# Kernel tuning notes

Measured on AMD Instinct MI355X. Metric: run time of the kernel, lower is better.

The kernel has to match this reference:

```python
import jax, jax.numpy as jnp
import numpy as np

N_HEAD = 16
D_K = 64


def _bn(x, g, b, eps=1e-5):
    # torch BatchNorm1d in training mode: biased batch variance
    m = jnp.mean(x, axis=0)
    v = jnp.var(x, axis=0)
    return (x - m) * jax.lax.rsqrt(v + eps) * g + b


def setup_inputs() -> dict:
    key = jax.random.key(0)
    ks = jax.random.split(key, 8)
    B, DX, NK, DKIN, H, DK, DO = 128, 1024, 1024, 512, N_HEAD, D_K, 512
    sc = 0.02
    return {
        "x": jax.random.normal(ks[0], (B, DX), dtype=jnp.float32),
        "k": jax.random.normal(ks[1], (B, NK, DKIN), dtype=jnp.float32),
        "bn1_g": jnp.ones((DX,), jnp.float32),
        "bn1_b": jnp.zeros((DX,), jnp.float32),
        "Wx": jax.random.normal(ks[2], (H * DK, DX), dtype=jnp.float32) * sc,
        "bx": jnp.zeros((H * DK,), jnp.float32),
        "Wk": jax.random.normal(ks[3], (H * DK, DKIN), dtype=jnp.float32) * sc,
        "bk": jnp.zeros((H * DK,), jnp.float32),
        "bn2_g": jnp.ones((DK,), jnp.float32),
        "bn2_b": jnp.zeros((DK,), jnp.float32),
        "Wlin": jax.random.normal(ks[4], (DK, DK), dtype=jnp.float32) * sc,
        "blin": jnp.zeros((DK,), jnp.float32),
        "Wo": jax.random.normal(ks[5], (DO, H * DK), dtype=jnp.float32) * sc,
        "bo": jnp.zeros((DO,), jnp.float32),
    }


def reference(x, k, bn1_g, bn1_b, Wx, bx, Wk, bk, bn2_g, bn2_b, Wlin, blin, Wo, bo):
    H, DK = N_HEAD, D_K
    B, DX = x.shape
    NK = k.shape[1]
    # outer BN + query projection (n_x == 1)
    xq = _bn(x, bn1_g, bn1_b) @ Wx.T + bx                     # (B, H*DK)
    xq = xq.reshape(B, H, DK).transpose(1, 0, 2).reshape(H * B, DK)
    kp = (k @ Wk.T + bk).reshape(B, NK, H, DK)
    kp = kp.transpose(2, 0, 1, 3).reshape(H * B, NK, DK)       # (H*B, NK, DK)
    # inner CrossAttention: BN + linear on the single query vector
    latent = _bn(xq, bn2_g, bn2_b) @ Wlin.T + blin             # (H*B, DK)
    u = jnp.einsum('bnd,bd->bn', kp, latent)                   # (H*B, NK)
    # softmax over the singleton query dim (dim=2) -> all ones, kept faithful
    attn = jax.nn.softmax(u[..., None], axis=-1)[..., 0]       # (H*B, NK)
    out = jnp.einsum('bnd,bn->bd', kp, attn)                   # (H*B, DK)
    out = out.reshape(H, B, DK).transpose(1, 0, 2).reshape(B, H * DK)
    x_hid = latent.reshape(H, B, DK).transpose(1, 0, 2).reshape(B, H * DK)
    # attn.view(n_head, batch, d_x_).permute(1,2,0).contiguous().view(batch, n_head, -1)
    attn_out = attn.reshape(H, B, NK).transpose(1, 2, 0).reshape(B, H, -1)
    return (attn_out, out @ Wo.T + bo, x_hid @ Wo.T + bo)
```

## Files before the change

### kernel.cpp

```cpp
#include <hip/hip_runtime.h>

typedef __attribute__((ext_vector_type(8))) short short8;
typedef __attribute__((ext_vector_type(4))) float floatx4;

__device__ __forceinline__ unsigned short f2bf(float f) {
    unsigned int x = __float_as_uint(f);
    x = x + 0x7FFFu + ((x >> 16) & 1u);
    return (unsigned short)(x >> 16);
}

template <typename OutT, bool STATS>
__device__ __forceinline__ void gemm_tile(
    const unsigned short* __restrict__ A, int lda,
    const unsigned short* __restrict__ B, int ldb,
    const float* __restrict__ bias, float bscale,
    OutT* __restrict__ C, int ldc, int tilesN, int K, int wave, int lane,
    float* sS, float* sSS)
{
    int tm = wave / tilesN, tn = wave % tilesN;
    int mn = lane & 15, q = lane >> 4;
    const short8* ap = (const short8*)(A + (size_t)(tm * 16 + mn) * lda + q * 8);
    const short8* bp = (const short8*)(B + (size_t)(tn * 16 + mn) * ldb + q * 8);
    floatx4 acc = {0.f, 0.f, 0.f, 0.f};
    #pragma unroll 4
    for (int k = 0; k < K; k += 32) {
        short8 a = *ap; ap += 4;
        short8 b = *bp; bp += 4;
        acc = __builtin_amdgcn_mfma_f32_16x16x32_bf16(a, b, acc, 0, 0, 0);
    }
    int col = tn * 16 + mn;
    float bv = bias[col] * bscale;
    float lsum = 0.f, lss = 0.f;
    #pragma unroll
    for (int r = 0; r < 4; ++r) {
        int row = tm * 16 + q * 4 + r;
        float v = acc[r] + bv;
        OutT* dst = C + (size_t)row * ldc + col;
        if constexpr (sizeof(OutT) == 2) *dst = (OutT)f2bf(v);
        else                             *dst = (OutT)v;
        if constexpr (STATS) { lsum += v; lss += v * v; }
    }
    if constexpr (STATS) {
        int d = col & 63;
        atomicAdd(&sS[d], lsum);
        atomicAdd(&sSS[d], lss);
    }
}

__global__ __launch_bounds__(256) void k_mega(
    const float* __restrict__ kk, float* __restrict__ part,
    const float* __restrict__ Wx, const float* __restrict__ Wk,
    const float* __restrict__ Wo, const float* __restrict__ Wl,
    unsigned short* __restrict__ Wxbf, unsigned short* __restrict__ Wkbf,
    unsigned short* __restrict__ Wobf, unsigned short* __restrict__ Wlbf,
    float4* __restrict__ attn_out,
    const float* __restrict__ x, const float* __restrict__ g1,
    const float* __restrict__ b1, unsigned short* __restrict__ xnbf,
    float* __restrict__ stats)
{
    int blk = blockIdx.x, tid = threadIdx.x;
    if (blk < 1024) {
        int b = blk >> 3, c = blk & 7;
        int f4 = tid & 127;
        int rh = tid >> 7;
        const float4* base = (const float4*)kk
            + ((size_t)(b * 1024 + c * 128 + rh) * 128 + f4);
        float4 acc = {0.f, 0.f, 0.f, 0.f};
        #pragma unroll 8
        for (int it = 0; it < 64; ++it) {
            float4 v = base[(size_t)it * 256];
            acc.x += v.x; acc.y += v.y; acc.z += v.z; acc.w += v.w;
        }
        __shared__ float red[2][512];
        red[rh][f4 * 4 + 0] = acc.x;
        red[rh][f4 * 4 + 1] = acc.y;
        red[rh][f4 * 4 + 2] = acc.z;
        red[rh][f4 * 4 + 3] = acc.w;
        __syncthreads();
        for (int j = tid; j < 512; j += 256)
            part[((size_t)(c * 128 + b) << 9) + j] = red[0][j] + red[1][j];
    } else if (blk < 3076) {
        int f = (blk - 1024) * 256 + tid;
        const float* src; unsigned short* dst; int off;
        if (f < 262144)      { src = Wx; dst = Wxbf; off = f; }
        else if (f < 393216) { src = Wk; dst = Wkbf; off = f - 262144; }
        else if (f < 524288) { src = Wo; dst = Wobf; off = f - 393216; }
        else                 { src = Wl; dst = Wlbf; off = f - 524288; }
        float4 v = ((const float4*)src)[off];
        uint2 o;
        o.x = (unsigned int)f2bf(v.x) | ((unsigned int)f2bf(v.y) << 16);
        o.y = (unsigned int)f2bf(v.z) | ((unsigned int)f2bf(v.w) << 16);
        *(uint2*)(dst + off * 4) = o;
    } else if (blk < 5124) {
        int idx = (blk - 3076) * 256 + tid;
        float4 ones = {1.f, 1.f, 1.f, 1.f};
        attn_out[idx] = ones;
    } else {
        if (blk == 5124 && tid < 128) stats[tid] = 0.f;
        int c = (blk - 5124) * 256 + tid;
        float s = 0.f, ss = 0.f;
        #pragma unroll 8
        for (int b = 0; b < 128; ++b) {
            float v = x[b * 1024 + c];
            s += v; ss += v * v;
        }
        float m  = s * (1.f / 128.f);
        float va = ss * (1.f / 128.f) - m * m;
        float rs = rsqrtf(va + 1e-5f);
        float a  = rs * g1[c];
        float b2 = b1[c] - m * a;
        #pragma unroll 8
        for (int b = 0; b < 128; ++b)
            xnbf[b * 1024 + c] = f2bf(x[b * 1024 + c] * a + b2);
    }
}

__global__ __launch_bounds__(128) void k_combine_xq(
    const float* __restrict__ part, unsigned short* __restrict__ ksumbf,
    const unsigned short* __restrict__ xnbf, const unsigned short* __restrict__ Wxbf,
    const float* __restrict__ bx, float* __restrict__ xq,
    float* __restrict__ stats)
{
    int blk = blockIdx.x, tid = threadIdx.x;
    if (blk < 64) {
        int idx = blk * 128 + tid;
        int b = idx >> 6;
        int j0 = (idx & 63) * 8;
        float s[8];
        #pragma unroll
        for (int u = 0; u < 8; ++u) s[u] = 0.f;
        #pragma unroll
        for (int c = 0; c < 8; ++c) {
            const float4* p = (const float4*)(part + ((size_t)(c * 128 + b) << 9) + j0);
            float4 a0 = p[0], a1 = p[1];
            s[0] += a0.x; s[1] += a0.y; s[2] += a0.z; s[3] += a0.w;
            s[4] += a1.x; s[5] += a1.y; s[6] += a1.z; s[7] += a1.w;
        }
        uint4 v;
        v.x = (unsigned int)f2bf(s[0]) | ((unsigned int)f2bf(s[1]) << 16);
        v.y = (unsigned int)f2bf(s[2]) | ((unsigned int)f2bf(s[3]) << 16);
        v.z = (unsigned int)f2bf(s[4]) | ((unsigned int)f2bf(s[5]) << 16);
        v.w = (unsigned int)f2bf(s[6]) | ((unsigned int)f2bf(s[7]) << 16);
        *(uint4*)(ksumbf + b * 512 + j0) = v;
    } else {
        __shared__ float sS[64], sSS[64];
        if (tid < 64) { sS[tid] = 0.f; sSS[tid] = 0.f; }
        __syncthreads();
        int wave = ((blk - 64) * 128 + tid) >> 6;
        gemm_tile<float, true>(xnbf, 1024, Wxbf, 1024, bx, 1.f, xq, 1024, 64, 1024,
                               wave, tid & 63, sS, sSS);
        __syncthreads();
        if (tid < 64)       atomicAdd(&stats[tid], sS[tid]);
        else                atomicAdd(&stats[tid], sSS[tid - 64]);
    }
}

__global__ __launch_bounds__(128) void k_outf_latent(
    const unsigned short* __restrict__ ksumbf, const unsigned short* __restrict__ Wkbf,
    const float* __restrict__ bk,
    const float* __restrict__ xq, const float* __restrict__ stats,
    const float* __restrict__ g2, const float* __restrict__ b2g,
    const unsigned short* __restrict__ Wlbf, const float* __restrict__ bl,
    unsigned short* __restrict__ concat)
{
    int blk = blockIdx.x, tid = threadIdx.x;
    if (blk < 256) {
        int wave = (blk * 128 + tid) >> 6;
        gemm_tile<unsigned short, false>(ksumbf, 512, Wkbf, 512, bk, 1024.f,
                                         concat, 1024, 64, 512, wave, tid & 63,
                                         nullptr, nullptr);
    } else {
        __shared__ float sa[64], sb[64];
        if (tid < 64) {
            float s = stats[tid], ss = stats[64 + tid];
            float m  = s * (1.f / 2048.f);
            float va = ss * (1.f / 2048.f) - m * m;
            float rs = rsqrtf(va + 1e-5f);
            float a  = rs * g2[tid];
            sa[tid] = a;
            sb[tid] = b2g[tid] - m * a;
        }
        __syncthreads();
        int w = tid >> 6, lane = tid & 63;
        int t = (blk - 256) * 2 + w;
        int tm = t >> 2, tn = t & 3;
        int mn = lane & 15, q = lane >> 4;
        const float4* xp = (const float4*)(xq + (size_t)tm * 1024 + mn * 64 + q * 8);
        const short8* bp = (const short8*)(Wlbf + (tn * 16 + mn) * 64 + q * 8);
        floatx4 acc = {0.f, 0.f, 0.f, 0.f};
        #pragma unroll
        for (int kk = 0; kk < 2; ++kk) {
            float4 x0 = xp[0], x1 = xp[1];
            xp += 8;
            int kb = kk * 32 + q * 8;
            short8 af;
            af[0] = (short)f2bf(x0.x * sa[kb + 0] + sb[kb + 0]);
            af[1] = (short)f2bf(x0.y * sa[kb + 1] + sb[kb + 1]);
            af[2] = (short)f2bf(x0.z * sa[kb + 2] + sb[kb + 2]);
            af[3] = (short)f2bf(x0.w * sa[kb + 3] + sb[kb + 3]);
            af[4] = (short)f2bf(x1.x * sa[kb + 4] + sb[kb + 4]);
            af[5] = (short)f2bf(x1.y * sa[kb + 5] + sb[kb + 5]);
            af[6] = (short)f2bf(x1.z * sa[kb + 6] + sb[kb + 6]);
            af[7] = (short)f2bf(x1.w * sa[kb + 7] + sb[kb + 7]);
            short8 bf = *bp; bp += 4;
            acc = __builtin_amdgcn_mfma_f32_16x16x32_bf16(af, bf, acc, 0, 0, 0);
        }
        int d = tn * 16 + mn;
        float bv = bl[d];
        #pragma unroll
        for (int r = 0; r < 4; ++r) {
            int h = q * 4 + r;
            concat[(size_t)(128 + tm) * 1024 + h * 64 + d] = f2bf(acc[r] + bv);
        }
    }
}

__global__ __launch_bounds__(128) void k_final_gemm(
    const unsigned short* __restrict__ concat, const unsigned short* __restrict__ Wobf,
    const float* __restrict__ bo, float* __restrict__ out12)
{
    int wave = (blockIdx.x * 128 + threadIdx.x) >> 6;
    gemm_tile<float, false>(concat, 1024, Wobf, 1024, bo, 1.f, out12, 512, 32, 1024,
                            wave, threadIdx.x & 63, nullptr, nullptr);
}

extern "C" void kernel_launch(void* const* d_in, const int* in_sizes, int n_in,
                              void* d_out, int out_size, void* d_ws, size_t ws_size,
                              hipStream_t stream) {
    (void)in_sizes; (void)n_in; (void)out_size; (void)ws_size;
    const float* x  = (const float*)d_in[0];
    const float* kk = (const float*)d_in[1];
    const float* g1 = (const float*)d_in[2];
    const float* b1 = (const float*)d_in[3];
    const float* Wx = (const float*)d_in[4];
    const float* bx = (const float*)d_in[5];
    const float* Wk = (const float*)d_in[6];
    const float* bk = (const float*)d_in[7];
    const float* g2 = (const float*)d_in[8];
    const float* b2 = (const float*)d_in[9];
    const float* Wl = (const float*)d_in[10];
    const float* bl = (const float*)d_in[11];
    const float* Wo = (const float*)d_in[12];
    const float* bo = (const float*)d_in[13];

    char* ws = (char*)d_ws;
    float*          part   = (float*)(ws + 0);
    unsigned short* Wxbf   = (unsigned short*)(ws + 2097152);
    unsigned short* Wkbf   = (unsigned short*)(ws + 4194304);
    unsigned short* Wobf   = (unsigned short*)(ws + 5242880);
    unsigned short* Wlbf   = (unsigned short*)(ws + 6291456);
    unsigned short* xnbf   = (unsigned short*)(ws + 6299648);
    unsigned short* ksumbf = (unsigned short*)(ws + 6561792);
    float*          xq     = (float*)(ws + 6692864);
    float*          stats  = (float*)(ws + 7217152);
    unsigned short* concat = (unsigned short*)(ws + 7217664);
    float*          out12  = (float*)d_out + 2097152;

    k_mega<<<5128, 256, 0, stream>>>(kk, part, Wx, Wk, Wo, Wl,
                                     Wxbf, Wkbf, Wobf, Wlbf,
                                     (float4*)d_out, x, g1, b1, xnbf, stats);
    k_combine_xq<<<320, 128, 0, stream>>>(part, ksumbf, xnbf, Wxbf, bx, xq, stats);
    k_outf_latent<<<512, 128, 0, stream>>>(ksumbf, Wkbf, bk, xq, stats,
                                           g2, b2, Wlbf, bl, concat);
    k_final_gemm<<<256, 128, 0, stream>>>(concat, Wobf, bo, out12);
}
```

Baseline: 419.4 us.

## Fuse out-projection, latent linear and final GEMM into one tail kernel via LDS

```diff
diff --git a/kernel.cpp b/kernel.cpp
--- a/kernel.cpp
+++ b/kernel.cpp
@@ -155,73 +155,121 @@
     }
 }
 
-__global__ __launch_bounds__(128) void k_outf_latent(
+__global__ __launch_bounds__(256) void k_tail(
     const unsigned short* __restrict__ ksumbf, const unsigned short* __restrict__ Wkbf,
     const float* __restrict__ bk,
     const float* __restrict__ xq, const float* __restrict__ stats,
     const float* __restrict__ g2, const float* __restrict__ b2g,
     const unsigned short* __restrict__ Wlbf, const float* __restrict__ bl,
-    unsigned short* __restrict__ concat)
+    const unsigned short* __restrict__ Wobf, const float* __restrict__ bo,
+    float* __restrict__ out12)
 {
+    __shared__ unsigned short ldsA[16][1032];
+    __shared__ unsigned short ldsB[16][1032];
+    __shared__ float sa[64], sbv[64];
     int blk = blockIdx.x, tid = threadIdx.x;
-    if (blk < 256) {
-        int wave = (blk * 128 + tid) >> 6;
-        gemm_tile<unsigned short, false>(ksumbf, 512, Wkbf, 512, bk, 1024.f,
-                                         concat, 1024, 64, 512, wave, tid & 63,
-                                         nullptr, nullptr);
-    } else {
-        __shared__ float sa[64], sb[64];
+    int tm = blk >> 1;
+    int wave = tid >> 6, lane = tid & 63;
+    int mn = lane & 15, q = lane >> 4;
+
+    if (blk & 1) {
         if (tid < 64) {
             float s = stats[tid], ss = stats[64 + tid];
             float m  = s * (1.f / 2048.f);
             float va = ss * (1.f / 2048.f) - m * m;
             float rs = rsqrtf(va + 1e-5f);
             float a  = rs * g2[tid];
-            sa[tid] = a;
-            sb[tid] = b2g[tid] - m * a;
-        }
-        __syncthreads();
-        int w = tid >> 6, lane = tid & 63;
-        int t = (blk - 256) * 2 + w;
-        int tm = t >> 2, tn = t & 3;
-        int mn = lane & 15, q = lane >> 4;
-        const float4* xp = (const float4*)(xq + (size_t)tm * 1024 + mn * 64 + q * 8);
-        const short8* bp = (const short8*)(Wlbf + (tn * 16 + mn) * 64 + q * 8);
-        floatx4 acc = {0.f, 0.f, 0.f, 0.f};
-        #pragma unroll
-        for (int kk = 0; kk < 2; ++kk) {
-            float4 x0 = xp[0], x1 = xp[1];
-            xp += 8;
-            int kb = kk * 32 + q * 8;
-            short8 af;
-            af[0] = (short)f2bf(x0.x * sa[kb + 0] + sb[kb + 0]);
-            af[1] = (short)f2bf(x0.y * sa[kb + 1] + sb[kb + 1]);
-            af[2] = (short)f2bf(x0.z * sa[kb + 2] + sb[kb + 2]);
-            af[3] = (short)f2bf(x0.w * sa[kb + 3] + sb[kb + 3]);
-            af[4] = (short)f2bf(x1.x * sa[kb + 4] + sb[kb + 4]);
-            af[5] = (short)f2bf(x1.y * sa[kb + 5] + sb[kb + 5]);
-            af[6] = (short)f2bf(x1.z * sa[kb + 6] + sb[kb + 6]);
-            af[7] = (short)f2bf(x1.w * sa[kb + 7] + sb[kb + 7]);
-            short8 bf = *bp; bp += 4;
-            acc = __builtin_amdgcn_mfma_f32_16x16x32_bf16(af, bf, acc, 0, 0, 0);
-        }
-        int d = tn * 16 + mn;
-        float bv = bl[d];
-        #pragma unroll
-        for (int r = 0; r < 4; ++r) {
-            int h = q * 4 + r;
-            concat[(size_t)(128 + tm) * 1024 + h * 64 + d] = f2bf(acc[r] + bv);
-        }
-    }
-}
-
-__global__ __launch_bounds__(128) void k_final_gemm(
-    const unsigned short* __restrict__ concat, const unsigned short* __restrict__ Wobf,
-    const float* __restrict__ bo, float* __restrict__ out12)
-{
-    int wave = (blockIdx.x * 128 + threadIdx.x) >> 6;
-    gemm_tile<float, false>(concat, 1024, Wobf, 1024, bo, 1.f, out12, 512, 32, 1024,
-                            wave, threadIdx.x & 63, nullptr, nullptr);
+            sa[tid]  = a;
+            sbv[tid] = b2g[tid] - m * a;
+        }
+        __syncthreads();
+        {
+            int row = tid & 15, cb = tid >> 4;
+            const float4* src = (const float4*)(xq + (size_t)(tm * 16 + row) * 1024 + cb * 64);
+            #pragma unroll
+            for (int i = 0; i < 8; ++i) {
+                float4 v0 = src[i * 2], v1 = src[i * 2 + 1];
+                short8 o;
+                o[0] = (short)f2bf(v0.x * sa[i * 8 + 0] + sbv[i * 8 + 0]);
+                o[1] = (short)f2bf(v0.y * sa[i * 8 + 1] + sbv[i * 8 + 1]);
+                o[2] = (short)f2bf(v0.z * sa[i * 8 + 2] + sbv[i * 8 + 2]);
+                o[3] = (short)f2bf(v0.w * sa[i * 8 + 3] + sbv[i * 8 + 3]);
+                o[4] = (short)f2bf(v1.x * sa[i * 8 + 4] + sbv[i * 8 + 4]);
+                o[5] = (short)f2bf(v1.y * sa[i * 8 + 5] + sbv[i * 8 + 5]);
+                o[6] = (short)f2bf(v1.z * sa[i * 8 + 6] + sbv[i * 8 + 6]);
+                o[7] = (short)f2bf(v1.w * sa[i * 8 + 7] + sbv[i * 8 + 7]);
+                *(short8*)&ldsA[row][cb * 64 + i * 8] = o;
+            }
+        }
+        __syncthreads();
+        #pragma unroll
+        for (int t = 0; t < 16; ++t) {
+            int h = wave * 4 + (t >> 2), tn = t & 3;
+            floatx4 acc = {0.f, 0.f, 0.f, 0.f};
+            #pragma unroll
+            for (int kk = 0; kk < 2; ++kk) {
+                short8 a = *(const short8*)&ldsA[mn][h * 64 + kk * 32 + q * 8];
+                short8 b = *(const short8*)(Wlbf + (size_t)(tn * 16 + mn) * 64 + kk * 32 + q * 8);
+                acc = __builtin_amdgcn_mfma_f32_16x16x32_bf16(a, b, acc, 0, 0, 0);
+            }
+            int d = tn * 16 + mn;
+            float bv = bl[d];
+            #pragma unroll
+            for (int r = 0; r < 4; ++r)
+                ldsB[q * 4 + r][h * 64 + d] = f2bf(acc[r] + bv);
+        }
+        __syncthreads();
+        #pragma unroll
+        for (int t = 0; t < 8; ++t) {
+            int tn = wave * 8 + t;
+            floatx4 acc = {0.f, 0.f, 0.f, 0.f};
+            #pragma unroll 8
+            for (int kk = 0; kk < 32; ++kk) {
+                short8 a = *(const short8*)&ldsB[mn][kk * 32 + q * 8];
+                short8 b = *(const short8*)(Wobf + (size_t)(tn * 16 + mn) * 1024 + kk * 32 + q * 8);
+                acc = __builtin_amdgcn_mfma_f32_16x16x32_bf16(a, b, acc, 0, 0, 0);
+            }
+            int col = tn * 16 + mn;
+            float bv = bo[col];
+            #pragma unroll
+            for (int r = 0; r < 4; ++r)
+                out12[(size_t)(128 + tm * 16 + q * 4 + r) * 512 + col] = acc[r] + bv;
+        }
+    } else {
+        #pragma unroll
+        for (int t = 0; t < 16; ++t) {
+            int tn = wave * 16 + t;
+            floatx4 acc = {0.f, 0.f, 0.f, 0.f};
+            #pragma unroll 4
+            for (int kk = 0; kk < 16; ++kk) {
+                short8 a = *(const short8*)(ksumbf + (size_t)(tm * 16 + mn) * 512 + kk * 32 + q * 8);
+                short8 b = *(const short8*)(Wkbf + (size_t)(tn * 16 + mn) * 512 + kk * 32 + q * 8);
+                acc = __builtin_amdgcn_mfma_f32_16x16x32_bf16(a, b, acc, 0, 0, 0);
+            }
+            int col = tn * 16 + mn;
+            float bv = bk[col] * 1024.f;
+            #pragma unroll
+            for (int r = 0; r < 4; ++r)
+                ldsA[q * 4 + r][col] = f2bf(acc[r] + bv);
+        }
+        __syncthreads();
+        #pragma unroll
+        for (int t = 0; t < 8; ++t) {
+            int tn = wave * 8 + t;
+            floatx4 acc = {0.f, 0.f, 0.f, 0.f};
+            #pragma unroll 8
+            for (int kk = 0; kk < 32; ++kk) {
+                short8 a = *(const short8*)&ldsA[mn][kk * 32 + q * 8];
+                short8 b = *(const short8*)(Wobf + (size_t)(tn * 16 + mn) * 1024 + kk * 32 + q * 8);
+                acc = __builtin_amdgcn_mfma_f32_16x16x32_bf16(a, b, acc, 0, 0, 0);
+            }
+            int col = tn * 16 + mn;
+            float bv = bo[col];
+            #pragma unroll
+            for (int r = 0; r < 4; ++r)
+                out12[(size_t)(tm * 16 + q * 4 + r) * 512 + col] = acc[r] + bv;
+        }
+    }
 }
 
 extern "C" void kernel_launch(void* const* d_in, const int* in_sizes, int n_in,
@@ -253,14 +301,12 @@
     unsigned short* ksumbf = (unsigned short*)(ws + 6561792);
     float*          xq     = (float*)(ws + 6692864);
     float*          stats  = (float*)(ws + 7217152);
-    unsigned short* concat = (unsigned short*)(ws + 7217664);
     float*          out12  = (float*)d_out + 2097152;
 
     k_mega<<<5128, 256, 0, stream>>>(kk, part, Wx, Wk, Wo, Wl,
                                      Wxbf, Wkbf, Wobf, Wlbf,
                                      (float4*)d_out, x, g1, b1, xnbf, stats);
     k_combine_xq<<<320, 128, 0, stream>>>(part, ksumbf, xnbf, Wxbf, bx, xq, stats);
-    k_outf_latent<<<512, 128, 0, stream>>>(ksumbf, Wkbf, bk, xq, stats,
-                                           g2, b2, Wlbf, bl, concat);
-    k_final_gemm<<<256, 128, 0, stream>>>(concat, Wobf, bo, out12);
-}
+    k_tail<<<16, 256, 0, stream>>>(ksumbf, Wkbf, bk, xq, stats,
+                                   g2, b2, Wlbf, bl, Wobf, bo, out12);
+}
```

Result: slower. 504.9 us (+20.4%).
